# Kernel optimization log

Hardware: AMD Instinct MI355X
Metric: run time of the kernel (lower is better)

## Reference

```python
import jax, jax.numpy as jnp
import numpy as np

HEADS = 4
DIM_HEAD = 128


def setup_inputs() -> dict:
    key = jax.random.key(0)
    k1, k2, k3 = jax.random.split(key, 3)
    dim = 256
    hidden = HEADS * DIM_HEAD  # 512
    x = jax.random.normal(k1, (16, dim, 64, 64), dtype=jnp.float32)
    # 1x1 conv weights stored as [out_ch, in_ch] (kernel dims squeezed)
    w_qkv = jax.random.normal(k2, (hidden * 3, dim), dtype=jnp.float32) * (1.0 / np.sqrt(dim))
    w_out = jax.random.normal(k3, (dim, hidden), dtype=jnp.float32) * (1.0 / np.sqrt(hidden))
    b_out = jnp.zeros((dim,), dtype=jnp.float32)
    return {"x": x, "w_qkv": w_qkv, "w_out": w_out, "b_out": b_out}


def reference(x, w_qkv, w_out, b_out):
    b, c, h, w = x.shape
    n = h * w
    # 1x1 conv == per-pixel linear projection
    qkv = jnp.einsum('bchw,oc->bohw', x, w_qkv)           # [b, 3*heads*dh, h, w]
    qkv = qkv.reshape(b, 3, HEADS, DIM_HEAD, n)           # 'b (qkv heads c) h w -> qkv b heads c (h w)'
    q, k, v = qkv[:, 0], qkv[:, 1], qkv[:, 2]             # [b, heads, dh, n]
    k = jax.nn.softmax(k, axis=-1)                        # softmax over spatial positions
    context = jnp.einsum('bhdn,bhen->bhde', k, v)         # [b, heads, dh, dh]
    out = jnp.einsum('bhde,bhdn->bhen', context, q)       # [b, heads, dh, n]
    out = out.reshape(b, HEADS * DIM_HEAD, h, w)          # 'b heads c (h w) -> b (heads c) h w'
    y = jnp.einsum('bchw,oc->bohw', out, w_out) + b_out[None, :, None, None]
    return y
```

## Files before the change

kernel.cpp:

```cpp
#include <hip/hip_runtime.h>

#define BATCH 16
#define CIN   256
#define NSP   4096
#define HID   512

typedef short v8s __attribute__((ext_vector_type(8)));
typedef float v4f __attribute__((ext_vector_type(4)));

__device__ __forceinline__ unsigned short f2bf(float f) {
    union { float f; unsigned u; } a; a.f = f;
    unsigned r = a.u + 0x7fffu + ((a.u >> 16) & 1u);
    return (unsigned short)(r >> 16);
}
__device__ __forceinline__ float bf2f(unsigned short s) {
    union { unsigned u; float f; } a; a.u = ((unsigned)s) << 16;
    return a.f;
}

__device__ __forceinline__ void gld_lds16(const unsigned short* g, unsigned short* l) {
    __builtin_amdgcn_global_load_lds(
        (const __attribute__((address_space(1))) unsigned int*)g,
        (__attribute__((address_space(3))) unsigned int*)l,
        16, 0, 0);
}

__global__ __launch_bounds__(256) void k_w(const float* __restrict__ wq,
                                           unsigned short* __restrict__ wbf,
                                           unsigned short* __restrict__ wqT) {
    const int bid = blockIdx.x;
    if (bid < 192) {
        const int t = bid * 256 + threadIdx.x;
        const float4 f0 = *(const float4*)(wq + (size_t)t * 8);
        const float4 f1 = *(const float4*)(wq + (size_t)t * 8 + 4);
        union { unsigned short s[8]; uint4 u; } p;
        p.s[0] = f2bf(f0.x); p.s[1] = f2bf(f0.y); p.s[2] = f2bf(f0.z); p.s[3] = f2bf(f0.w);
        p.s[4] = f2bf(f1.x); p.s[5] = f2bf(f1.y); p.s[6] = f2bf(f1.z); p.s[7] = f2bf(f1.w);
        *(uint4*)(wbf + (size_t)t * 8) = p.u;
        return;
    }
    __shared__ float tile[64 * 65];
    const int bb = bid - 192;
    const int u0 = (bb & 7) * 64, c0 = (bb >> 3) * 64;
    const int t = threadIdx.x;
    {
        const int cl = (t & 15) * 4, ul = t >> 4;
        #pragma unroll
        for (int i = 0; i < 4; i++) {
            int u = ul + i * 16;
            const float4 f = *(const float4*)(wq + (size_t)(u0 + u) * CIN + c0 + cl);
            *(float4*)(&tile[u * 65 + cl]) = f;
        }
    }
    __syncthreads();
    {
        const int ul4 = (t & 15) * 4, cl = t >> 4;
        #pragma unroll
        for (int i = 0; i < 4; i++) {
            int c = cl + i * 16;
            union { unsigned short s[4]; uint2 u; } p;
            #pragma unroll
            for (int j = 0; j < 4; j++)
                p.s[j] = f2bf(tile[(ul4 + j) * 65 + c]);
            *(uint2*)(wqT + (size_t)(c0 + c) * HID + u0 + ul4) = p.u;
        }
    }
}

__global__ __launch_bounds__(256) void k_prep(const float* __restrict__ x,
                                              unsigned short* __restrict__ xbf,
                                              unsigned short* __restrict__ xT) {
    __shared__ float tile[64 * 65];
    const int t = threadIdx.x;
    const int n0 = blockIdx.x * 64, c0 = blockIdx.y * 64, bz = blockIdx.z;
    const float* xb = x + (size_t)bz * CIN * NSP;
    {
        const int nl = (t & 15) * 4, cl = t >> 4;
        #pragma unroll
        for (int i = 0; i < 4; i++) {
            int c = cl + i * 16;
            const float4 f = *(const float4*)(xb + (size_t)(c0 + c) * NSP + n0 + nl);
            *(float4*)(&tile[c * 65 + nl]) = f;
            union { unsigned short s[4]; uint2 u; } p;
            p.s[0] = f2bf(f.x); p.s[1] = f2bf(f.y); p.s[2] = f2bf(f.z); p.s[3] = f2bf(f.w);
            *(uint2*)(xbf + ((size_t)bz * CIN + c0 + c) * NSP + n0 + nl) = p.u;
        }
    }
    __syncthreads();
    {
        const int cl4 = (t & 15) * 4, nl = t >> 4;
        #pragma unroll
        for (int i = 0; i < 4; i++) {
            int n = nl + i * 16;
            union { unsigned short s[4]; uint2 u; } p;
            #pragma unroll
            for (int j = 0; j < 4; j++)
                p.s[j] = f2bf(tile[(cl4 + j) * 65 + n]);
            *(uint2*)(xT + ((size_t)bz * NSP + n0 + n) * CIN + c0 + cl4) = p.u;
        }
    }
}

__global__ __launch_bounds__(256) void k_k(const unsigned short* __restrict__ wbf,
                                           const unsigned short* __restrict__ xT,
                                           unsigned short* __restrict__ expk,
                                           float* __restrict__ zp) {
    __shared__ __align__(16) unsigned short As[128 * 32];
    __shared__ __align__(16) unsigned short Bs[128 * 32];
    const int t = threadIdx.x;
    const int id = blockIdx.x;
    const int bz = id >> 7;
    const int r  = id & 127;
    const int xcd = r & 7, s = r >> 3;
    const int bn = (xcd << 2) | (s & 3);
    const int bm = s >> 2;
    const int d0 = bm * 128, n0 = bn * 128;
    const int lane = t & 63, wv = t >> 6;
    const int quad = lane >> 4, l15 = lane & 15;
    const int wmN = (wv & 1) * 64, wnD = (wv >> 1) * 64;

    const int srow = lane >> 2, scol = (lane & 3) * 8;
    unsigned short* Al0 = As + wv * 16 * 32;
    unsigned short* Al1 = Al0 + 64 * 32;
    unsigned short* Bl0 = Bs + wv * 16 * 32;
    unsigned short* Bl1 = Bl0 + 64 * 32;
    const unsigned short* Ag0 = xT + ((size_t)bz * NSP + n0 + wv * 16 + srow) * CIN + scol;
    const unsigned short* Ag1 = Ag0 + 64 * CIN;
    const unsigned short* Bg0 = wbf + (size_t)(512 + d0 + wv * 16 + srow) * CIN + scol;
    const unsigned short* Bg1 = Bg0 + 64 * CIN;

    v4f acc[4][4];
    #pragma unroll
    for (int i = 0; i < 4; i++)
        #pragma unroll
        for (int j = 0; j < 4; j++) acc[i][j] = (v4f)0.f;

    for (int kk = 0; kk < CIN; kk += 32) {
        gld_lds16(Ag0 + kk, Al0);
        gld_lds16(Ag1 + kk, Al1);
        gld_lds16(Bg0 + kk, Bl0);
        gld_lds16(Bg1 + kk, Bl1);
        __syncthreads();
        v8s af[4], bfr[4];
        #pragma unroll
        for (int mi = 0; mi < 4; mi++) {
            union { v8s v; uint4 u; } rr;
            rr.u = *(const uint4*)(&As[(wmN + mi * 16 + l15) * 32 + quad * 8]);
            af[mi] = rr.v;
        }
        #pragma unroll
        for (int ni = 0; ni < 4; ni++) {
            union { v8s v; uint4 u; } rr;
            rr.u = *(const uint4*)(&Bs[(wnD + ni * 16 + l15) * 32 + quad * 8]);
            bfr[ni] = rr.v;
        }
        #pragma unroll
        for (int mi = 0; mi < 4; mi++)
            #pragma unroll
            for (int ni = 0; ni < 4; ni++)
                acc[mi][ni] = __builtin_amdgcn_mfma_f32_16x16x32_bf16(af[mi], bfr[ni], acc[mi][ni], 0, 0, 0);
        __syncthreads();
    }

    float zacc[4] = {0.f, 0.f, 0.f, 0.f};
    #pragma unroll
    for (int ni = 0; ni < 4; ni++) {
        const int d = d0 + wnD + ni * 16 + l15;
        #pragma unroll
        for (int mi = 0; mi < 4; mi++) {
            const int nb = n0 + wmN + mi * 16 + quad * 4;
            union { unsigned short s[4]; uint2 u; } p;
            #pragma unroll
            for (int rr = 0; rr < 4; rr++) {
                float e = __expf(acc[mi][ni][rr]);
                zacc[ni] += e;
                p.s[rr] = f2bf(e);
            }
            *(uint2*)(expk + ((size_t)bz * 512 + d) * NSP + nb) = p.u;
        }
    }
    #pragma unroll
    for (int ni = 0; ni < 4; ni++) {
        float z = zacc[ni];
        z += __shfl_xor(z, 16);
        z += __shfl_xor(z, 32);
        if (quad == 0)
            zp[((size_t)bz * 512 + d0 + wnD + ni * 16 + l15) * 64 + bn * 2 + (wv & 1)] = z;
    }
}

__global__ __launch_bounds__(256) void k_S(const unsigned short* __restrict__ expk,
                                           const unsigned short* __restrict__ xbf,
                                           float* __restrict__ Sp) {
    __shared__ __align__(16) unsigned short As[128 * 32];
    __shared__ __align__(16) unsigned short Bs[128 * 32];
    const int t = threadIdx.x;
    const int id = blockIdx.x;
    const int hc = id >> 6;
    const int h = hc >> 1, ch = hc & 1;
    const int bkc = id & 63;
    const int b = bkc >> 2, kc = bkc & 3;
    const int kw = kc * 1024;
    const int lane = t & 63, wv = t >> 6, quad = lane >> 4, l15 = lane & 15;
    const int wmC = (wv & 1) * 64, wnD = (wv >> 1) * 64;

    const int srow = lane >> 2, scol = (lane & 3) * 8;
    unsigned short* Al0 = As + wv * 16 * 32;
    unsigned short* Al1 = Al0 + 64 * 32;
    unsigned short* Bl0 = Bs + wv * 16 * 32;
    unsigned short* Bl1 = Bl0 + 64 * 32;
    const unsigned short* Ag0 = xbf + ((size_t)b * CIN + ch * 128 + wv * 16 + srow) * NSP + kw + scol;
    const unsigned short* Ag1 = Ag0 + 64 * NSP;
    const unsigned short* Bg0 = expk + ((size_t)b * 512 + h * 128 + wv * 16 + srow) * NSP + kw + scol;
    const unsigned short* Bg1 = Bg0 + 64 * NSP;

    v4f acc[4][4];
    #pragma unroll
    for (int i = 0; i < 4; i++)
        #pragma unroll
        for (int j = 0; j < 4; j++) acc[i][j] = (v4f)0.f;

    for (int kk = 0; kk < 1024; kk += 32) {
        gld_lds16(Ag0 + kk, Al0);
        gld_lds16(Ag1 + kk, Al1);
        gld_lds16(Bg0 + kk, Bl0);
        gld_lds16(Bg1 + kk, Bl1);
        __syncthreads();
        v8s af[4], bfr[4];
        #pragma unroll
        for (int mi = 0; mi < 4; mi++) {
            union { v8s v; uint4 u; } rr;
            rr.u = *(const uint4*)(&As[(wmC + mi * 16 + l15) * 32 + quad * 8]);
            af[mi] = rr.v;
        }
        #pragma unroll
        for (int ni = 0; ni < 4; ni++) {
            union { v8s v; uint4 u; } rr;
            rr.u = *(const uint4*)(&Bs[(wnD + ni * 16 + l15) * 32 + quad * 8]);
            bfr[ni] = rr.v;
        }
        #pragma unroll
        for (int mi = 0; mi < 4; mi++)
            #pragma unroll
            for (int ni = 0; ni < 4; ni++)
                acc[mi][ni] = __builtin_amdgcn_mfma_f32_16x16x32_bf16(af[mi], bfr[ni], acc[mi][ni], 0, 0, 0);
        __syncthreads();
    }

    const int bh = b * 4 + h;
    float* outp = Sp + ((size_t)(bh * 2 + ch) * 4 + kc) * 16384;
    #pragma unroll
    for (int ni = 0; ni < 4; ni++) {
        const int d = wnD + ni * 16 + l15;
        #pragma unroll
        for (int mi = 0; mi < 4; mi++) {
            const int c = wmC + mi * 16 + quad * 4;
            *(v4f*)(outp + d * 128 + c) = acc[mi][ni];
        }
    }
}

__global__ __launch_bounds__(256) void k_sred(const float* __restrict__ Sp,
                                              unsigned short* __restrict__ Sred) {
    const int qv = blockIdx.x * 256 + threadIdx.x;
    const int bh = qv >> 13, r = qv & 8191;
    const int dl = r >> 6, cq6 = r & 63;
    const int ch = cq6 >> 5, clq = cq6 & 31;
    const float* p = Sp + ((size_t)(bh * 2 + ch) * 4) * 16384 + dl * 128 + clq * 4;
    float4 s = *(const float4*)p;
    #pragma unroll
    for (int kc = 1; kc < 4; kc++) {
        const float4 f = *(const float4*)(p + (size_t)kc * 16384);
        s.x += f.x; s.y += f.y; s.z += f.z; s.w += f.w;
    }
    union { unsigned short us[4]; uint2 u; } pk;
    pk.us[0] = f2bf(s.x); pk.us[1] = f2bf(s.y); pk.us[2] = f2bf(s.z); pk.us[3] = f2bf(s.w);
    *(uint2*)(Sred + (size_t)bh * 32768 + dl * 256 + cq6 * 4) = pk.u;
}

__global__ __launch_bounds__(256) void k_redwc(const unsigned short* __restrict__ Sred,
                                               const float* __restrict__ zp,
                                               const unsigned short* __restrict__ wbf,
                                               const float* __restrict__ w_out,
                                               unsigned short* __restrict__ Wc) {
    __shared__ unsigned short Ds[128 * 136];
    __shared__ float zinv[128];
    const int t = threadIdx.x;
    const int bh = blockIdx.x;  const int b = bh >> 2, h = bh & 3;
    const int lane = t & 63, wv = t >> 6, quad = lane >> 4, l15 = lane & 15;

    if (t < 128) {
        float z = 0.f;
        #pragma unroll
        for (int nt = 0; nt < 64; nt++)
            z += zp[((size_t)b * 512 + h * 128 + t) * 64 + nt];
        zinv[t] = 1.0f / z;
    }
    __syncthreads();

    {
        const int wm = (wv & 1) * 64, wn = (wv >> 1) * 64;
        const unsigned short* Sb = Sred + (size_t)bh * 32768;
        const unsigned short* Vb = wbf + (size_t)(1024 + h * 128) * CIN;
        v4f acc[4][4];
        #pragma unroll
        for (int i = 0; i < 4; i++)
            #pragma unroll
            for (int j = 0; j < 4; j++) acc[i][j] = (v4f)0.f;
        for (int kk = 0; kk < CIN; kk += 32) {
            v8s af[4], bfr[4];
            #pragma unroll
            for (int mi = 0; mi < 4; mi++) {
                union { v8s v; uint4 u; } rr;
                rr.u = *(const uint4*)(Sb + (size_t)(wm + mi * 16 + l15) * 256 + kk + quad * 8);
                af[mi] = rr.v;
            }
            #pragma unroll
            for (int ni = 0; ni < 4; ni++) {
                union { v8s v; uint4 u; } rr;
                rr.u = *(const uint4*)(Vb + (size_t)(wn + ni * 16 + l15) * 256 + kk + quad * 8);
                bfr[ni] = rr.v;
            }
            #pragma unroll
            for (int mi = 0; mi < 4; mi++)
                #pragma unroll
                for (int ni = 0; ni < 4; ni++)
                    acc[mi][ni] = __builtin_amdgcn_mfma_f32_16x16x32_bf16(af[mi], bfr[ni], acc[mi][ni], 0, 0, 0);
        }
        float zq[4][4];
        #pragma unroll
        for (int mi = 0; mi < 4; mi++)
            #pragma unroll
            for (int rr = 0; rr < 4; rr++)
                zq[mi][rr] = zinv[wm + mi * 16 + quad * 4 + rr];
        #pragma unroll
        for (int mi = 0; mi < 4; mi++)
            #pragma unroll
            for (int ni = 0; ni < 4; ni++)
                #pragma unroll
                for (int rr = 0; rr < 4; rr++)
                    Ds[(wm + mi * 16 + quad * 4 + rr) * 136 + wn + ni * 16 + l15] =
                        f2bf(acc[mi][ni][rr] * zq[mi][rr]);
    }
    __syncthreads();

    {
        const int wm = wv * 64;
        v4f acc[4][8];
        #pragma unroll
        for (int i = 0; i < 4; i++)
            #pragma unroll
            for (int j = 0; j < 8; j++) acc[i][j] = (v4f)0.f;
        for (int kk = 0; kk < 128; kk += 32) {
            v8s af[4], bfr[8];
            #pragma unroll
            for (int mi = 0; mi < 4; mi++) {
                int o = wm + mi * 16 + l15;
                const float* wp = w_out + (size_t)o * HID + h * 128 + kk + quad * 8;
                float4 f0 = *(const float4*)wp;
                float4 f1 = *(const float4*)(wp + 4);
                union { v8s v; unsigned short s[8]; } r;
                r.s[0] = f2bf(f0.x); r.s[1] = f2bf(f0.y); r.s[2] = f2bf(f0.z); r.s[3] = f2bf(f0.w);
                r.s[4] = f2bf(f1.x); r.s[5] = f2bf(f1.y); r.s[6] = f2bf(f1.z); r.s[7] = f2bf(f1.w);
                af[mi] = r.v;
            }
            #pragma unroll
            for (int ni = 0; ni < 8; ni++) {
                const unsigned short* p = &Ds[(ni * 16 + l15) * 136 + kk + quad * 8];
                union { v8s v; uint4 u; } r;
                r.u = *(const uint4*)p;
                bfr[ni] = r.v;
            }
            #pragma unroll
            for (int mi = 0; mi < 4; mi++)
                #pragma unroll
                for (int ni = 0; ni < 8; ni++)
                    acc[mi][ni] = __builtin_amdgcn_mfma_f32_16x16x32_bf16(af[mi], bfr[ni], acc[mi][ni], 0, 0, 0);
        }
        #pragma unroll
        for (int ni = 0; ni < 8; ni++) {
            int d = ni * 16 + l15;
            #pragma unroll
            for (int mi = 0; mi < 4; mi++)
                #pragma unroll
                for (int rr = 0; rr < 4; rr++) {
                    int o = wm + mi * 16 + quad * 4 + rr;
                    Wc[((size_t)b * 256 + o) * HID + h * 128 + d] = f2bf(acc[mi][ni][rr]);
                }
        }
    }
}

__global__ __launch_bounds__(256) void k_chain(const unsigned short* __restrict__ Wc,
                                               const unsigned short* __restrict__ wqT,
                                               unsigned short* __restrict__ Weff) {
    __shared__ __align__(16) unsigned short As[128 * 32];
    __shared__ __align__(16) unsigned short Bs[128 * 32];
    const int t = threadIdx.x;
    const int c0 = blockIdx.x * 128, o0 = blockIdx.y * 128, bz = blockIdx.z;
    const int lane = t & 63, wv = t >> 6, quad = lane >> 4, l15 = lane & 15;
    const int wmC = (wv & 1) * 64, wnO = (wv >> 1) * 64;

    const int srow = lane >> 2, scol = (lane & 3) * 8;
    unsigned short* Al0 = As + wv * 16 * 32;
    unsigned short* Al1 = Al0 + 64 * 32;
    unsigned short* Bl0 = Bs + wv * 16 * 32;
    unsigned short* Bl1 = Bl0 + 64 * 32;
    const unsigned short* Ag0 = wqT + (size_t)(c0 + wv * 16 + srow) * HID + scol;
    const unsigned short* Ag1 = Ag0 + 64 * HID;
    const unsigned short* Bg0 = Wc + ((size_t)bz * 256 + o0 + wv * 16 + srow) * HID + scol;
    const unsigned short* Bg1 = Bg0 + 64 * HID;

    v4f acc[4][4];
    #pragma unroll
    for (int i = 0; i < 4; i++)
        #pragma unroll
        for (int j = 0; j < 4; j++) acc[i][j] = (v4f)0.f;

    for (int kk = 0; kk < HID; kk += 32) {
        gld_lds16(Ag0 + kk, Al0);
        gld_lds16(Ag1 + kk, Al1);
        gld_lds16(Bg0 + kk, Bl0);
        gld_lds16(Bg1 + kk, Bl1);
        __syncthreads();
        v8s af[4], bfr[4];
        #pragma unroll
        for (int mi = 0; mi < 4; mi++) {
            union { v8s v; uint4 u; } rr;
            rr.u = *(const uint4*)(&As[(wmC + mi * 16 + l15) * 32 + quad * 8]);
            af[mi] = rr.v;
        }
        #pragma unroll
        for (int ni = 0; ni < 4; ni++) {
            union { v8s v; uint4 u; } rr;
            rr.u = *(const uint4*)(&Bs[(wnO + ni * 16 + l15) * 32 + quad * 8]);
            bfr[ni] = rr.v;
        }
        #pragma unroll
        for (int mi = 0; mi < 4; mi++)
            #pragma unroll
            for (int ni = 0; ni < 4; ni++)
                acc[mi][ni] = __builtin_amdgcn_mfma_f32_16x16x32_bf16(af[mi], bfr[ni], acc[mi][ni], 0, 0, 0);
        __syncthreads();
    }
    #pragma unroll
    for (int ni = 0; ni < 4; ni++) {
        const int o = o0 + wnO + ni * 16 + l15;
        #pragma unroll
        for (int mi = 0; mi < 4; mi++) {
            const int c = c0 + wmC + mi * 16 + quad * 4;
            union { unsigned short s[4]; uint2 u; } p;
            #pragma unroll
            for (int rr = 0; rr < 4; rr++) p.s[rr] = f2bf(acc[mi][ni][rr]);
            *(uint2*)(Weff + ((size_t)bz * 256 + o) * 256 + c) = p.u;
        }
    }
}

__global__ __launch_bounds__(256) void k_y(const unsigned short* __restrict__ Weff,
                                           const unsigned short* __restrict__ xT,
                                           const float* __restrict__ b_out,
                                           float* __restrict__ y) {
    __shared__ __align__(16) unsigned short As[128 * 32];
    __shared__ __align__(16) unsigned short Bs[128 * 32];
    const int t = threadIdx.x;
    const int o0 = blockIdx.x * 128;
    const int n0 = blockIdx.y * 128;
    const int bz = blockIdx.z;
    const int lane = t & 63, wv = t >> 6, quad = lane >> 4, l15 = lane & 15;
    const int wmN = (wv & 1) * 64, wnO = (wv >> 1) * 64;

    const int srow = lane >> 2, scol = (lane & 3) * 8;
    unsigned short* Al0 = As + wv * 16 * 32;
    unsigned short* Al1 = Al0 + 64 * 32;
    unsigned short* Bl0 = Bs + wv * 16 * 32;
    unsigned short* Bl1 = Bl0 + 64 * 32;
    const unsigned short* Ag0 = xT + ((size_t)bz * NSP + n0 + wv * 16 + srow) * CIN + scol;
    const unsigned short* Ag1 = Ag0 + 64 * CIN;
    const unsigned short* Bg0 = Weff + ((size_t)bz * 256 + o0 + wv * 16 + srow) * CIN + scol;
    const unsigned short* Bg1 = Bg0 + 64 * CIN;

    v4f acc[4][4];
    #pragma unroll
    for (int i = 0; i < 4; i++)
        #pragma unroll
        for (int j = 0; j < 4; j++) acc[i][j] = (v4f)0.f;

    for (int kk = 0; kk < CIN; kk += 32) {
        gld_lds16(Ag0 + kk, Al0);
        gld_lds16(Ag1 + kk, Al1);
        gld_lds16(Bg0 + kk, Bl0);
        gld_lds16(Bg1 + kk, Bl1);
        __syncthreads();
        v8s af[4], bfr[4];
        #pragma unroll
        for (int mi = 0; mi < 4; mi++) {
            union { v8s v; uint4 u; } rr;
            rr.u = *(const uint4*)(&As[(wmN + mi * 16 + l15) * 32 + quad * 8]);
            af[mi] = rr.v;
        }
        #pragma unroll
        for (int ni = 0; ni < 4; ni++) {
            union { v8s v; uint4 u; } rr;
            rr.u = *(const uint4*)(&Bs[(wnO + ni * 16 + l15) * 32 + quad * 8]);
            bfr[ni] = rr.v;
        }
        #pragma unroll
        for (int mi = 0; mi < 4; mi++)
            #pragma unroll
            for (int ni = 0; ni < 4; ni++)
                acc[mi][ni] = __builtin_amdgcn_mfma_f32_16x16x32_bf16(af[mi], bfr[ni], acc[mi][ni], 0, 0, 0);
        __syncthreads();
    }
    #pragma unroll
    for (int ni = 0; ni < 4; ni++) {
        const int o = o0 + wnO + ni * 16 + l15;
        const float bias = b_out[o];
        #pragma unroll
        for (int mi = 0; mi < 4; mi++) {
            const int n = n0 + wmN + mi * 16 + quad * 4;
            v4f v = acc[mi][ni];
            v[0] += bias; v[1] += bias; v[2] += bias; v[3] += bias;
            *(v4f*)(y + ((size_t)bz * 256 + o) * NSP + n) = v;
        }
    }
}

extern "C" void kernel_launch(void* const* d_in, const int* in_sizes, int n_in,
                              void* d_out, int out_size, void* d_ws, size_t ws_size,
                              hipStream_t stream) {
    (void)in_sizes; (void)n_in; (void)out_size; (void)ws_size;
    const float* x     = (const float*)d_in[0];
    const float* w_qkv = (const float*)d_in[1];
    const float* w_out = (const float*)d_in[2];
    const float* b_out = (const float*)d_in[3];
    float* y = (float*)d_out;
    char* ws = (char*)d_ws;

    unsigned short* xT   = (unsigned short*)(ws);
    unsigned short* xbf  = (unsigned short*)(ws + 33554432);
    unsigned short* expk = (unsigned short*)(ws + 67108864);
    float*          Sp   = (float*)(ws + 134217728);
    float*          zp   = (float*)(ws + 167772160);
    unsigned short* Sred = (unsigned short*)(ws + 176160768);
    unsigned short* Wc   = (unsigned short*)(ws + 180355072);
    unsigned short* Weff = (unsigned short*)(ws + 184549376);
    unsigned short* wbf  = (unsigned short*)(ws + 186646528);
    unsigned short* wqT  = (unsigned short*)(ws + 187432960);

    k_w    <<<dim3(224),        256, 0, stream>>>(w_qkv, wbf, wqT);
    k_prep <<<dim3(64, 4, 16),  256, 0, stream>>>(x, xbf, xT);
    k_k    <<<dim3(2048),       256, 0, stream>>>(wbf, xT, expk, zp);
    k_S    <<<dim3(512),        256, 0, stream>>>(expk, xbf, Sp);
    k_sred <<<dim3(2048),       256, 0, stream>>>(Sp, Sred);
    k_redwc<<<dim3(64),         256, 0, stream>>>(Sred, zp, wbf, w_out, Wc);
    k_chain<<<dim3(2, 2, 16),   256, 0, stream>>>(Wc, wqT, Weff);
    k_y    <<<dim3(2, 32, 16),  256, 0, stream>>>(Weff, xT, b_out, y);
}
```

Measured before the change: 259.6 us.

## Merge prep kernels, atomically accumulate partial sums, and use swizzled 64-wide K tiles

Folds the weight-conversion kernel and the zeroing of accumulators into one prep launch. The k-softmax denominators and the k_S partial context products now go straight into fp32 buffers through atomicAdd, which removes the separate k_sred reduction kernel and its scratch traffic. All GEMM kernels move to K-tiles of 64 with an XOR-style swizzled LDS layout, meant to halve barrier count and avoid bank conflicts. In exchange the code relies on ordering between kernels for the zeroing and accepts contention from fp32 atomics, whose summation order is nondeterministic.

```diff
diff --git a/kernel.cpp b/kernel.cpp
--- a/kernel.cpp
+++ b/kernel.cpp
@@ -12,10 +12,6 @@
     union { float f; unsigned u; } a; a.f = f;
     unsigned r = a.u + 0x7fffu + ((a.u >> 16) & 1u);
     return (unsigned short)(r >> 16);
-}
-__device__ __forceinline__ float bf2f(unsigned short s) {
-    union { unsigned u; float f; } a; a.u = ((unsigned)s) << 16;
-    return a.f;
 }
 
 __device__ __forceinline__ void gld_lds16(const unsigned short* g, unsigned short* l) {
@@ -25,54 +21,61 @@
         16, 0, 0);
 }
 
-__global__ __launch_bounds__(256) void k_w(const float* __restrict__ wq,
-                                           unsigned short* __restrict__ wbf,
-                                           unsigned short* __restrict__ wqT) {
+
+__global__ __launch_bounds__(256) void k_prep(const float* __restrict__ x,
+                                              const float* __restrict__ wq,
+                                              unsigned short* __restrict__ xbf,
+                                              unsigned short* __restrict__ xT,
+                                              unsigned short* __restrict__ wbf,
+                                              unsigned short* __restrict__ wqT,
+                                              float* __restrict__ zacc) {
     const int bid = blockIdx.x;
-    if (bid < 192) {
-        const int t = bid * 256 + threadIdx.x;
-        const float4 f0 = *(const float4*)(wq + (size_t)t * 8);
-        const float4 f1 = *(const float4*)(wq + (size_t)t * 8 + 4);
-        union { unsigned short s[8]; uint4 u; } p;
-        p.s[0] = f2bf(f0.x); p.s[1] = f2bf(f0.y); p.s[2] = f2bf(f0.z); p.s[3] = f2bf(f0.w);
-        p.s[4] = f2bf(f1.x); p.s[5] = f2bf(f1.y); p.s[6] = f2bf(f1.z); p.s[7] = f2bf(f1.w);
-        *(uint4*)(wbf + (size_t)t * 8) = p.u;
+    const int t = threadIdx.x;
+    if (bid >= 4320) {
+        zacc[(bid - 4320) * 256 + t] = 0.f;
         return;
     }
+    if (bid >= 4096) {
+        const int wid = bid - 4096;
+        if (wid < 192) {
+            const int g = wid * 256 + t;
+            const float4 f0 = *(const float4*)(wq + (size_t)g * 8);
+            const float4 f1 = *(const float4*)(wq + (size_t)g * 8 + 4);
+            union { unsigned short s[8]; uint4 u; } p;
+            p.s[0] = f2bf(f0.x); p.s[1] = f2bf(f0.y); p.s[2] = f2bf(f0.z); p.s[3] = f2bf(f0.w);
+            p.s[4] = f2bf(f1.x); p.s[5] = f2bf(f1.y); p.s[6] = f2bf(f1.z); p.s[7] = f2bf(f1.w);
+            *(uint4*)(wbf + (size_t)g * 8) = p.u;
+            return;
+        }
+        __shared__ float tile[64 * 65];
+        const int bb = wid - 192;
+        const int u0 = (bb & 7) * 64, c0 = (bb >> 3) * 64;
+        {
+            const int cl = (t & 15) * 4, ul = t >> 4;
+            #pragma unroll
+            for (int i = 0; i < 4; i++) {
+                int u = ul + i * 16;
+                const float4 f = *(const float4*)(wq + (size_t)(u0 + u) * CIN + c0 + cl);
+                *(float4*)(&tile[u * 65 + cl]) = f;
+            }
+        }
+        __syncthreads();
+        {
+            const int ul4 = (t & 15) * 4, cl = t >> 4;
+            #pragma unroll
+            for (int i = 0; i < 4; i++) {
+                int c = cl + i * 16;
+                union { unsigned short s[4]; uint2 u; } p;
+                #pragma unroll
+                for (int j = 0; j < 4; j++)
+                    p.s[j] = f2bf(tile[(ul4 + j) * 65 + c]);
+                *(uint2*)(wqT + (size_t)(c0 + c) * HID + u0 + ul4) = p.u;
+            }
+        }
+        return;
+    }
     __shared__ float tile[64 * 65];
-    const int bb = bid - 192;
-    const int u0 = (bb & 7) * 64, c0 = (bb >> 3) * 64;
-    const int t = threadIdx.x;
-    {
-        const int cl = (t & 15) * 4, ul = t >> 4;
-        #pragma unroll
-        for (int i = 0; i < 4; i++) {
-            int u = ul + i * 16;
-            const float4 f = *(const float4*)(wq + (size_t)(u0 + u) * CIN + c0 + cl);
-            *(float4*)(&tile[u * 65 + cl]) = f;
-        }
-    }
-    __syncthreads();
-    {
-        const int ul4 = (t & 15) * 4, cl = t >> 4;
-        #pragma unroll
-        for (int i = 0; i < 4; i++) {
-            int c = cl + i * 16;
-            union { unsigned short s[4]; uint2 u; } p;
-            #pragma unroll
-            for (int j = 0; j < 4; j++)
-                p.s[j] = f2bf(tile[(ul4 + j) * 65 + c]);
-            *(uint2*)(wqT + (size_t)(c0 + c) * HID + u0 + ul4) = p.u;
-        }
-    }
-}
-
-__global__ __launch_bounds__(256) void k_prep(const float* __restrict__ x,
-                                              unsigned short* __restrict__ xbf,
-                                              unsigned short* __restrict__ xT) {
-    __shared__ float tile[64 * 65];
-    const int t = threadIdx.x;
-    const int n0 = blockIdx.x * 64, c0 = blockIdx.y * 64, bz = blockIdx.z;
+    const int n0 = (bid & 63) * 64, c0 = ((bid >> 6) & 3) * 64, bz = bid >> 8;
     const float* xb = x + (size_t)bz * CIN * NSP;
     {
         const int nl = (t & 15) * 4, cl = t >> 4;
@@ -104,30 +107,32 @@
 __global__ __launch_bounds__(256) void k_k(const unsigned short* __restrict__ wbf,
                                            const unsigned short* __restrict__ xT,
                                            unsigned short* __restrict__ expk,
-                                           float* __restrict__ zp) {
-    __shared__ __align__(16) unsigned short As[128 * 32];
-    __shared__ __align__(16) unsigned short Bs[128 * 32];
+                                           float* __restrict__ zacc,
+                                           float* __restrict__ Sacc) {
+    __shared__ __align__(16) unsigned short As[128 * 64];
+    __shared__ __align__(16) unsigned short Bs[128 * 64];
     const int t = threadIdx.x;
     const int id = blockIdx.x;
+    ((float4*)Sacc)[(size_t)id * 256 + t] = make_float4(0.f, 0.f, 0.f, 0.f);
+
     const int bz = id >> 7;
-    const int r  = id & 127;
-    const int xcd = r & 7, s = r >> 3;
-    const int bn = (xcd << 2) | (s & 3);
-    const int bm = s >> 2;
+    const int r7 = id & 127;
+    const int xcd = r7 & 7, s7 = r7 >> 3;
+    const int bn = (xcd << 2) | (s7 & 3);
+    const int bm = s7 >> 2;
     const int d0 = bm * 128, n0 = bn * 128;
     const int lane = t & 63, wv = t >> 6;
     const int quad = lane >> 4, l15 = lane & 15;
     const int wmN = (wv & 1) * 64, wnD = (wv >> 1) * 64;
 
-    const int srow = lane >> 2, scol = (lane & 3) * 8;
-    unsigned short* Al0 = As + wv * 16 * 32;
-    unsigned short* Al1 = Al0 + 64 * 32;
-    unsigned short* Bl0 = Bs + wv * 16 * 32;
-    unsigned short* Bl1 = Bl0 + 64 * 32;
-    const unsigned short* Ag0 = xT + ((size_t)bz * NSP + n0 + wv * 16 + srow) * CIN + scol;
-    const unsigned short* Ag1 = Ag0 + 64 * CIN;
-    const unsigned short* Bg0 = wbf + (size_t)(512 + d0 + wv * 16 + srow) * CIN + scol;
-    const unsigned short* Bg1 = Bg0 + 64 * CIN;
+    const int srow8 = lane >> 3, sslot = lane & 7;
+    const int scol = ((sslot - srow8) & 7) * 8;
+    const int sw0 = ((quad + l15) & 7) * 8;
+
+    const unsigned short* Ag = xT + ((size_t)bz * NSP + n0 + wv * 32 + srow8) * CIN + scol;
+    const unsigned short* Bg = wbf + (size_t)(512 + d0 + wv * 32 + srow8) * CIN + scol;
+    unsigned short* Al = As + wv * 32 * 64;
+    unsigned short* Bl = Bs + wv * 32 * 64;
 
     v4f acc[4][4];
     #pragma unroll
@@ -135,34 +140,39 @@
         #pragma unroll
         for (int j = 0; j < 4; j++) acc[i][j] = (v4f)0.f;
 
-    for (int kk = 0; kk < CIN; kk += 32) {
-        gld_lds16(Ag0 + kk, Al0);
-        gld_lds16(Ag1 + kk, Al1);
-        gld_lds16(Bg0 + kk, Bl0);
-        gld_lds16(Bg1 + kk, Bl1);
-        __syncthreads();
-        v8s af[4], bfr[4];
-        #pragma unroll
-        for (int mi = 0; mi < 4; mi++) {
-            union { v8s v; uint4 u; } rr;
-            rr.u = *(const uint4*)(&As[(wmN + mi * 16 + l15) * 32 + quad * 8]);
-            af[mi] = rr.v;
-        }
-        #pragma unroll
-        for (int ni = 0; ni < 4; ni++) {
-            union { v8s v; uint4 u; } rr;
-            rr.u = *(const uint4*)(&Bs[(wnD + ni * 16 + l15) * 32 + quad * 8]);
-            bfr[ni] = rr.v;
-        }
-        #pragma unroll
-        for (int mi = 0; mi < 4; mi++)
-            #pragma unroll
-            for (int ni = 0; ni < 4; ni++)
-                acc[mi][ni] = __builtin_amdgcn_mfma_f32_16x16x32_bf16(af[mi], bfr[ni], acc[mi][ni], 0, 0, 0);
-        __syncthreads();
-    }
-
-    float zacc[4] = {0.f, 0.f, 0.f, 0.f};
+    for (int kk = 0; kk < CIN; kk += 64) {
+        #pragma unroll
+        for (int cc = 0; cc < 4; cc++) {
+            gld_lds16(Ag + (size_t)(cc * 8) * CIN + kk, Al + cc * 8 * 64);
+            gld_lds16(Bg + (size_t)(cc * 8) * CIN + kk, Bl + cc * 8 * 64);
+        }
+        __syncthreads();
+        #pragma unroll
+        for (int h = 0; h < 2; h++) {
+            const int sw = sw0 ^ (h * 32);
+            v8s af[4], bfr[4];
+            #pragma unroll
+            for (int mi = 0; mi < 4; mi++) {
+                union { v8s v; uint4 u; } rr;
+                rr.u = *(const uint4*)(&As[(wmN + mi * 16 + l15) * 64 + sw]);
+                af[mi] = rr.v;
+            }
+            #pragma unroll
+            for (int ni = 0; ni < 4; ni++) {
+                union { v8s v; uint4 u; } rr;
+                rr.u = *(const uint4*)(&Bs[(wnD + ni * 16 + l15) * 64 + sw]);
+                bfr[ni] = rr.v;
+            }
+            #pragma unroll
+            for (int mi = 0; mi < 4; mi++)
+                #pragma unroll
+                for (int ni = 0; ni < 4; ni++)
+                    acc[mi][ni] = __builtin_amdgcn_mfma_f32_16x16x32_bf16(af[mi], bfr[ni], acc[mi][ni], 0, 0, 0);
+        }
+        __syncthreads();
+    }
+
+    float za[4] = {0.f, 0.f, 0.f, 0.f};
     #pragma unroll
     for (int ni = 0; ni < 4; ni++) {
         const int d = d0 + wnD + ni * 16 + l15;
@@ -173,7 +183,7 @@
             #pragma unroll
             for (int rr = 0; rr < 4; rr++) {
                 float e = __expf(acc[mi][ni][rr]);
-                zacc[ni] += e;
+                za[ni] += e;
                 p.s[rr] = f2bf(e);
             }
             *(uint2*)(expk + ((size_t)bz * 512 + d) * NSP + nb) = p.u;
@@ -181,19 +191,19 @@
     }
     #pragma unroll
     for (int ni = 0; ni < 4; ni++) {
-        float z = zacc[ni];
+        float z = za[ni];
         z += __shfl_xor(z, 16);
         z += __shfl_xor(z, 32);
         if (quad == 0)
-            zp[((size_t)bz * 512 + d0 + wnD + ni * 16 + l15) * 64 + bn * 2 + (wv & 1)] = z;
+            atomicAdd(&zacc[bz * 512 + d0 + wnD + ni * 16 + l15], z);
     }
 }
 
 __global__ __launch_bounds__(256) void k_S(const unsigned short* __restrict__ expk,
                                            const unsigned short* __restrict__ xbf,
-                                           float* __restrict__ Sp) {
-    __shared__ __align__(16) unsigned short As[128 * 32];
-    __shared__ __align__(16) unsigned short Bs[128 * 32];
+                                           float* __restrict__ Sacc) {
+    __shared__ __align__(16) unsigned short As[128 * 64];
+    __shared__ __align__(16) unsigned short Bs[128 * 64];
     const int t = threadIdx.x;
     const int id = blockIdx.x;
     const int hc = id >> 6;
@@ -204,15 +214,14 @@
     const int lane = t & 63, wv = t >> 6, quad = lane >> 4, l15 = lane & 15;
     const int wmC = (wv & 1) * 64, wnD = (wv >> 1) * 64;
 
-    const int srow = lane >> 2, scol = (lane & 3) * 8;
-    unsigned short* Al0 = As + wv * 16 * 32;
-    unsigned short* Al1 = Al0 + 64 * 32;
-    unsigned short* Bl0 = Bs + wv * 16 * 32;
-    unsigned short* Bl1 = Bl0 + 64 * 32;
-    const unsigned short* Ag0 = xbf + ((size_t)b * CIN + ch * 128 + wv * 16 + srow) * NSP + kw + scol;
-    const unsigned short* Ag1 = Ag0 + 64 * NSP;
-    const unsigned short* Bg0 = expk + ((size_t)b * 512 + h * 128 + wv * 16 + srow) * NSP + kw + scol;
-    const unsigned short* Bg1 = Bg0 + 64 * NSP;
+    const int srow8 = lane >> 3, sslot = lane & 7;
+    const int scol = ((sslot - srow8) & 7) * 8;
+    const int sw0 = ((quad + l15) & 7) * 8;
+
+    const unsigned short* Ag = xbf + ((size_t)b * CIN + ch * 128 + wv * 32 + srow8) * NSP + kw + scol;
+    const unsigned short* Bg = expk + ((size_t)b * 512 + h * 128 + wv * 32 + srow8) * NSP + kw + scol;
+    unsigned short* Al = As + wv * 32 * 64;
+    unsigned short* Bl = Bs + wv * 32 * 64;
 
     v4f acc[4][4];
     #pragma unroll
@@ -220,66 +229,55 @@
         #pragma unroll
         for (int j = 0; j < 4; j++) acc[i][j] = (v4f)0.f;
 
-    for (int kk = 0; kk < 1024; kk += 32) {
-        gld_lds16(Ag0 + kk, Al0);
-        gld_lds16(Ag1 + kk, Al1);
-        gld_lds16(Bg0 + kk, Bl0);
-        gld_lds16(Bg1 + kk, Bl1);
-        __syncthreads();
-        v8s af[4], bfr[4];
-        #pragma unroll
-        for (int mi = 0; mi < 4; mi++) {
-            union { v8s v; uint4 u; } rr;
-            rr.u = *(const uint4*)(&As[(wmC + mi * 16 + l15) * 32 + quad * 8]);
-            af[mi] = rr.v;
-        }
-        #pragma unroll
-        for (int ni = 0; ni < 4; ni++) {
-            union { v8s v; uint4 u; } rr;
-            rr.u = *(const uint4*)(&Bs[(wnD + ni * 16 + l15) * 32 + quad * 8]);
-            bfr[ni] = rr.v;
-        }
-        #pragma unroll
-        for (int mi = 0; mi < 4; mi++)
-            #pragma unroll
-            for (int ni = 0; ni < 4; ni++)
-                acc[mi][ni] = __builtin_amdgcn_mfma_f32_16x16x32_bf16(af[mi], bfr[ni], acc[mi][ni], 0, 0, 0);
+    for (int kk = 0; kk < 1024; kk += 64) {
+        #pragma unroll
+        for (int cc = 0; cc < 4; cc++) {
+            gld_lds16(Ag + (size_t)(cc * 8) * NSP + kk, Al + cc * 8 * 64);
+            gld_lds16(Bg + (size_t)(cc * 8) * NSP + kk, Bl + cc * 8 * 64);
+        }
+        __syncthreads();
+        #pragma unroll
+        for (int h2 = 0; h2 < 2; h2++) {
+            const int sw = sw0 ^ (h2 * 32);
+            v8s af[4], bfr[4];
+            #pragma unroll
+            for (int mi = 0; mi < 4; mi++) {
+                union { v8s v; uint4 u; } rr;
+                rr.u = *(const uint4*)(&As[(wmC + mi * 16 + l15) * 64 + sw]);
+                af[mi] = rr.v;
+            }
+            #pragma unroll
+            for (int ni = 0; ni < 4; ni++) {
+                union { v8s v; uint4 u; } rr;
+                rr.u = *(const uint4*)(&Bs[(wnD + ni * 16 + l15) * 64 + sw]);
+                bfr[ni] = rr.v;
+            }
+            #pragma unroll
+            for (int mi = 0; mi < 4; mi++)
+                #pragma unroll
+                for (int ni = 0; ni < 4; ni++)
+                    acc[mi][ni] = __builtin_amdgcn_mfma_f32_16x16x32_bf16(af[mi], bfr[ni], acc[mi][ni], 0, 0, 0);
+        }
         __syncthreads();
     }
 
     const int bh = b * 4 + h;
-    float* outp = Sp + ((size_t)(bh * 2 + ch) * 4 + kc) * 16384;
+    float* outp = Sacc + (size_t)bh * 32768;
     #pragma unroll
     for (int ni = 0; ni < 4; ni++) {
         const int d = wnD + ni * 16 + l15;
         #pragma unroll
         for (int mi = 0; mi < 4; mi++) {
-            const int c = wmC + mi * 16 + quad * 4;
-            *(v4f*)(outp + d * 128 + c) = acc[mi][ni];
-        }
-    }
-}
-
-__global__ __launch_bounds__(256) void k_sred(const float* __restrict__ Sp,
-                                              unsigned short* __restrict__ Sred) {
-    const int qv = blockIdx.x * 256 + threadIdx.x;
-    const int bh = qv >> 13, r = qv & 8191;
-    const int dl = r >> 6, cq6 = r & 63;
-    const int ch = cq6 >> 5, clq = cq6 & 31;
-    const float* p = Sp + ((size_t)(bh * 2 + ch) * 4) * 16384 + dl * 128 + clq * 4;
-    float4 s = *(const float4*)p;
-    #pragma unroll
-    for (int kc = 1; kc < 4; kc++) {
-        const float4 f = *(const float4*)(p + (size_t)kc * 16384);
-        s.x += f.x; s.y += f.y; s.z += f.z; s.w += f.w;
-    }
-    union { unsigned short us[4]; uint2 u; } pk;
-    pk.us[0] = f2bf(s.x); pk.us[1] = f2bf(s.y); pk.us[2] = f2bf(s.z); pk.us[3] = f2bf(s.w);
-    *(uint2*)(Sred + (size_t)bh * 32768 + dl * 256 + cq6 * 4) = pk.u;
-}
-
-__global__ __launch_bounds__(256) void k_redwc(const unsigned short* __restrict__ Sred,
-                                               const float* __restrict__ zp,
+            const int c = ch * 128 + wmC + mi * 16 + quad * 4;
+            #pragma unroll
+            for (int rr = 0; rr < 4; rr++)
+                atomicAdd(&outp[d * 256 + c + rr], acc[mi][ni][rr]);
+        }
+    }
+}
+
+__global__ __launch_bounds__(256) void k_redwc(const float* __restrict__ Sacc,
+                                               const float* __restrict__ zacc,
                                                const unsigned short* __restrict__ wbf,
                                                const float* __restrict__ w_out,
                                                unsigned short* __restrict__ Wc) {
@@ -289,18 +287,12 @@
     const int bh = blockIdx.x;  const int b = bh >> 2, h = bh & 3;
     const int lane = t & 63, wv = t >> 6, quad = lane >> 4, l15 = lane & 15;
 
-    if (t < 128) {
-        float z = 0.f;
-        #pragma unroll
-        for (int nt = 0; nt < 64; nt++)
-            z += zp[((size_t)b * 512 + h * 128 + t) * 64 + nt];
-        zinv[t] = 1.0f / z;
-    }
+    if (t < 128) zinv[t] = 1.0f / zacc[b * 512 + h * 128 + t];
     __syncthreads();
 
     {
         const int wm = (wv & 1) * 64, wn = (wv >> 1) * 64;
-        const unsigned short* Sb = Sred + (size_t)bh * 32768;
+        const float* Sb = Sacc + (size_t)bh * 32768;
         const unsigned short* Vb = wbf + (size_t)(1024 + h * 128) * CIN;
         v4f acc[4][4];
         #pragma unroll
@@ -311,9 +303,13 @@
             v8s af[4], bfr[4];
             #pragma unroll
             for (int mi = 0; mi < 4; mi++) {
-                union { v8s v; uint4 u; } rr;
-                rr.u = *(const uint4*)(Sb + (size_t)(wm + mi * 16 + l15) * 256 + kk + quad * 8);
-                af[mi] = rr.v;
+                const float* sp = Sb + (size_t)(wm + mi * 16 + l15) * 256 + kk + quad * 8;
+                float4 f0 = *(const float4*)sp;
+                float4 f1 = *(const float4*)(sp + 4);
+                union { v8s v; unsigned short s[8]; } r;
+                r.s[0] = f2bf(f0.x); r.s[1] = f2bf(f0.y); r.s[2] = f2bf(f0.z); r.s[3] = f2bf(f0.w);
+                r.s[4] = f2bf(f1.x); r.s[5] = f2bf(f1.y); r.s[6] = f2bf(f1.z); r.s[7] = f2bf(f1.w);
+                af[mi] = r.v;
             }
             #pragma unroll
             for (int ni = 0; ni < 4; ni++) {
@@ -366,9 +362,8 @@
             }
             #pragma unroll
             for (int ni = 0; ni < 8; ni++) {
-                const unsigned short* p = &Ds[(ni * 16 + l15) * 136 + kk + quad * 8];
                 union { v8s v; uint4 u; } r;
-                r.u = *(const uint4*)p;
+                r.u = *(const uint4*)(&Ds[(ni * 16 + l15) * 136 + kk + quad * 8]);
                 bfr[ni] = r.v;
             }
             #pragma unroll
@@ -394,22 +389,21 @@
 __global__ __launch_bounds__(256) void k_chain(const unsigned short* __restrict__ Wc,
                                                const unsigned short* __restrict__ wqT,
                                                unsigned short* __restrict__ Weff) {
-    __shared__ __align__(16) unsigned short As[128 * 32];
-    __shared__ __align__(16) unsigned short Bs[128 * 32];
+    __shared__ __align__(16) unsigned short As[128 * 64];
+    __shared__ __align__(16) unsigned short Bs[128 * 64];
     const int t = threadIdx.x;
     const int c0 = blockIdx.x * 128, o0 = blockIdx.y * 128, bz = blockIdx.z;
     const int lane = t & 63, wv = t >> 6, quad = lane >> 4, l15 = lane & 15;
     const int wmC = (wv & 1) * 64, wnO = (wv >> 1) * 64;
 
-    const int srow = lane >> 2, scol = (lane & 3) * 8;
-    unsigned short* Al0 = As + wv * 16 * 32;
-    unsigned short* Al1 = Al0 + 64 * 32;
-    unsigned short* Bl0 = Bs + wv * 16 * 32;
-    unsigned short* Bl1 = Bl0 + 64 * 32;
-    const unsigned short* Ag0 = wqT + (size_t)(c0 + wv * 16 + srow) * HID + scol;
-    const unsigned short* Ag1 = Ag0 + 64 * HID;
-    const unsigned short* Bg0 = Wc + ((size_t)bz * 256 + o0 + wv * 16 + srow) * HID + scol;
-    const unsigned short* Bg1 = Bg0 + 64 * HID;
+    const int srow8 = lane >> 3, sslot = lane & 7;
+    const int scol = ((sslot - srow8) & 7) * 8;
+    const int sw0 = ((quad + l15) & 7) * 8;
+
+    const unsigned short* Ag = wqT + (size_t)(c0 + wv * 32 + srow8) * HID + scol;
+    const unsigned short* Bg = Wc + ((size_t)bz * 256 + o0 + wv * 32 + srow8) * HID + scol;
+    unsigned short* Al = As + wv * 32 * 64;
+    unsigned short* Bl = Bs + wv * 32 * 64;
 
     v4f acc[4][4];
     #pragma unroll
@@ -417,30 +411,35 @@
         #pragma unroll
         for (int j = 0; j < 4; j++) acc[i][j] = (v4f)0.f;
 
-    for (int kk = 0; kk < HID; kk += 32) {
-        gld_lds16(Ag0 + kk, Al0);
-        gld_lds16(Ag1 + kk, Al1);
-        gld_lds16(Bg0 + kk, Bl0);
-        gld_lds16(Bg1 + kk, Bl1);
-        __syncthreads();
-        v8s af[4], bfr[4];
-        #pragma unroll
-        for (int mi = 0; mi < 4; mi++) {
-            union { v8s v; uint4 u; } rr;
-            rr.u = *(const uint4*)(&As[(wmC + mi * 16 + l15) * 32 + quad * 8]);
-            af[mi] = rr.v;
-        }
-        #pragma unroll
-        for (int ni = 0; ni < 4; ni++) {
-            union { v8s v; uint4 u; } rr;
-            rr.u = *(const uint4*)(&Bs[(wnO + ni * 16 + l15) * 32 + quad * 8]);
-            bfr[ni] = rr.v;
-        }
-        #pragma unroll
-        for (int mi = 0; mi < 4; mi++)
-            #pragma unroll
-            for (int ni = 0; ni < 4; ni++)
-                acc[mi][ni] = __builtin_amdgcn_mfma_f32_16x16x32_bf16(af[mi], bfr[ni], acc[mi][ni], 0, 0, 0);
+    for (int kk = 0; kk < HID; kk += 64) {
+        #pragma unroll
+        for (int cc = 0; cc < 4; cc++) {
+            gld_lds16(Ag + (size_t)(cc * 8) * HID + kk, Al + cc * 8 * 64);
+            gld_lds16(Bg + (size_t)(cc * 8) * HID + kk, Bl + cc * 8 * 64);
+        }
+        __syncthreads();
+        #pragma unroll
+        for (int h = 0; h < 2; h++) {
+            const int sw = sw0 ^ (h * 32);
+            v8s af[4], bfr[4];
+            #pragma unroll
+            for (int mi = 0; mi < 4; mi++) {
+                union { v8s v; uint4 u; } rr;
+                rr.u = *(const uint4*)(&As[(wmC + mi * 16 + l15) * 64 + sw]);
+                af[mi] = rr.v;
+            }
+            #pragma unroll
+            for (int ni = 0; ni < 4; ni++) {
+                union { v8s v; uint4 u; } rr;
+                rr.u = *(const uint4*)(&Bs[(wnO + ni * 16 + l15) * 64 + sw]);
+                bfr[ni] = rr.v;
+            }
+            #pragma unroll
+            for (int mi = 0; mi < 4; mi++)
+                #pragma unroll
+                for (int ni = 0; ni < 4; ni++)
+                    acc[mi][ni] = __builtin_amdgcn_mfma_f32_16x16x32_bf16(af[mi], bfr[ni], acc[mi][ni], 0, 0, 0);
+        }
         __syncthreads();
     }
     #pragma unroll
@@ -461,8 +460,8 @@
                                            const unsigned short* __restrict__ xT,
                                            const float* __restrict__ b_out,
                                            float* __restrict__ y) {
-    __shared__ __align__(16) unsigned short As[128 * 32];
-    __shared__ __align__(16) unsigned short Bs[128 * 32];
+    __shared__ __align__(16) unsigned short As[128 * 64];
+    __shared__ __align__(16) unsigned short Bs[128 * 64];
     const int t = threadIdx.x;
     const int o0 = blockIdx.x * 128;
     const int n0 = blockIdx.y * 128;
@@ -470,15 +469,14 @@
     const int lane = t & 63, wv = t >> 6, quad = lane >> 4, l15 = lane & 15;
     const int wmN = (wv & 1) * 64, wnO = (wv >> 1) * 64;
 
-    const int srow = lane >> 2, scol = (lane & 3) * 8;
-    unsigned short* Al0 = As + wv * 16 * 32;
-    unsigned short* Al1 = Al0 + 64 * 32;
-    unsigned short* Bl0 = Bs + wv * 16 * 32;
-    unsigned short* Bl1 = Bl0 + 64 * 32;
-    const unsigned short* Ag0 = xT + ((size_t)bz * NSP + n0 + wv * 16 + srow) * CIN + scol;
-    const unsigned short* Ag1 = Ag0 + 64 * CIN;
-    const unsigned short* Bg0 = Weff + ((size_t)bz * 256 + o0 + wv * 16 + srow) * CIN + scol;
-    const unsigned short* Bg1 = Bg0 + 64 * CIN;
+    const int srow8 = lane >> 3, sslot = lane & 7;
+    const int scol = ((sslot - srow8) & 7) * 8;
+    const int sw0 = ((quad + l15) & 7) * 8;
+
+    const unsigned short* Ag = xT + ((size_t)bz * NSP + n0 + wv * 32 + srow8) * CIN + scol;
+    const unsigned short* Bg = Weff + ((size_t)bz * 256 + o0 + wv * 32 + srow8) * CIN + scol;
+    unsigned short* Al = As + wv * 32 * 64;
+    unsigned short* Bl = Bs + wv * 32 * 64;
 
     v4f acc[4][4];
     #pragma unroll
@@ -486,30 +484,35 @@
         #pragma unroll
         for (int j = 0; j < 4; j++) acc[i][j] = (v4f)0.f;
 
-    for (int kk = 0; kk < CIN; kk += 32) {
-        gld_lds16(Ag0 + kk, Al0);
-        gld_lds16(Ag1 + kk, Al1);
-        gld_lds16(Bg0 + kk, Bl0);
-        gld_lds16(Bg1 + kk, Bl1);
-        __syncthreads();
-        v8s af[4], bfr[4];
-        #pragma unroll
-        for (int mi = 0; mi < 4; mi++) {
-            union { v8s v; uint4 u; } rr;
-            rr.u = *(const uint4*)(&As[(wmN + mi * 16 + l15) * 32 + quad * 8]);
-            af[mi] = rr.v;
-        }
-        #pragma unroll
-        for (int ni = 0; ni < 4; ni++) {
-            union { v8s v; uint4 u; } rr;
-            rr.u = *(const uint4*)(&Bs[(wnO + ni * 16 + l15) * 32 + quad * 8]);
-            bfr[ni] = rr.v;
-        }
-        #pragma unroll
-        for (int mi = 0; mi < 4; mi++)
-            #pragma unroll
-            for (int ni = 0; ni < 4; ni++)
-                acc[mi][ni] = __builtin_amdgcn_mfma_f32_16x16x32_bf16(af[mi], bfr[ni], acc[mi][ni], 0, 0, 0);
+    for (int kk = 0; kk < CIN; kk += 64) {
+        #pragma unroll
+        for (int cc = 0; cc < 4; cc++) {
+            gld_lds16(Ag + (size_t)(cc * 8) * CIN + kk, Al + cc * 8 * 64);
+            gld_lds16(Bg + (size_t)(cc * 8) * CIN + kk, Bl + cc * 8 * 64);
+        }
+        __syncthreads();
+        #pragma unroll
+        for (int h = 0; h < 2; h++) {
+            const int sw = sw0 ^ (h * 32);
+            v8s af[4], bfr[4];
+            #pragma unroll
+            for (int mi = 0; mi < 4; mi++) {
+                union { v8s v; uint4 u; } rr;
+                rr.u = *(const uint4*)(&As[(wmN + mi * 16 + l15) * 64 + sw]);
+                af[mi] = rr.v;
+            }
+            #pragma unroll
+            for (int ni = 0; ni < 4; ni++) {
+                union { v8s v; uint4 u; } rr;
+                rr.u = *(const uint4*)(&Bs[(wnO + ni * 16 + l15) * 64 + sw]);
+                bfr[ni] = rr.v;
+            }
+            #pragma unroll
+            for (int mi = 0; mi < 4; mi++)
+                #pragma unroll
+                for (int ni = 0; ni < 4; ni++)
+                    acc[mi][ni] = __builtin_amdgcn_mfma_f32_16x16x32_bf16(af[mi], bfr[ni], acc[mi][ni], 0, 0, 0);
+        }
         __syncthreads();
     }
     #pragma unroll
@@ -540,20 +543,17 @@
     unsigned short* xT   = (unsigned short*)(ws);
     unsigned short* xbf  = (unsigned short*)(ws + 33554432);
     unsigned short* expk = (unsigned short*)(ws + 67108864);
-    float*          Sp   = (float*)(ws + 134217728);
-    float*          zp   = (float*)(ws + 167772160);
-    unsigned short* Sred = (unsigned short*)(ws + 176160768);
-    unsigned short* Wc   = (unsigned short*)(ws + 180355072);
-    unsigned short* Weff = (unsigned short*)(ws + 184549376);
-    unsigned short* wbf  = (unsigned short*)(ws + 186646528);
-    unsigned short* wqT  = (unsigned short*)(ws + 187432960);
-
-    k_w    <<<dim3(224),        256, 0, stream>>>(w_qkv, wbf, wqT);
-    k_prep <<<dim3(64, 4, 16),  256, 0, stream>>>(x, xbf, xT);
-    k_k    <<<dim3(2048),       256, 0, stream>>>(wbf, xT, expk, zp);
-    k_S    <<<dim3(512),        256, 0, stream>>>(expk, xbf, Sp);
-    k_sred <<<dim3(2048),       256, 0, stream>>>(Sp, Sred);
-    k_redwc<<<dim3(64),         256, 0, stream>>>(Sred, zp, wbf, w_out, Wc);
+    float*          Sacc = (float*)(ws + 134217728);
+    float*          zacc = (float*)(ws + 142606336);
+    unsigned short* Wc   = (unsigned short*)(ws + 142639104);
+    unsigned short* Weff = (unsigned short*)(ws + 146833408);
+    unsigned short* wbf  = (unsigned short*)(ws + 148930560);
+    unsigned short* wqT  = (unsigned short*)(ws + 149716992);
+
+    k_prep <<<dim3(4352),       256, 0, stream>>>(x, w_qkv, xbf, xT, wbf, wqT, zacc);
+    k_k    <<<dim3(2048),       256, 0, stream>>>(wbf, xT, expk, zacc, Sacc);
+    k_S    <<<dim3(512),        256, 0, stream>>>(expk, xbf, Sacc);
+    k_redwc<<<dim3(64),         256, 0, stream>>>(Sacc, zacc, wbf, w_out, Wc);
     k_chain<<<dim3(2, 2, 16),   256, 0, stream>>>(Wc, wqT, Weff);
     k_y    <<<dim3(2, 32, 16),  256, 0, stream>>>(Weff, xT, b_out, y);
 }
```

Measured after the change: 336.8 us. 29.7% more time.
